# Kernel optimization log

Measured on AMD Instinct MI355X. Metric: run time of the kernel, lower is better.

Reference implementation:

```python
import jax, jax.numpy as jnp
import numpy as np

H = 90            # hidden_size (hard-coded in module)
NODE_F = 16       # conv1 in_channels = dim(x) + dim(pos)
EDGE_F = 8
N_GRAPHS = 512


def _init_linear(key, fan_in, fan_out):
    kw, kb = jax.random.split(key)
    bound = 1.0 / np.sqrt(fan_in)
    w = jax.random.uniform(kw, (fan_in, fan_out), minval=-bound, maxval=bound, dtype=jnp.float32)
    b = jax.random.uniform(kb, (fan_out,), minval=-bound, maxval=bound, dtype=jnp.float32)
    return w, b


def setup_inputs() -> dict:
    key = jax.random.key(0)
    ks = jax.random.split(key, 16)
    N, E = 16000, 64000
    x = jax.random.normal(ks[0], (N, 13), dtype=jnp.float32)
    pos = jax.random.normal(ks[1], (N, 3), dtype=jnp.float32)
    edge_attr = jax.random.normal(ks[2], (E, EDGE_F), dtype=jnp.float32)
    edge_index = jax.random.randint(ks[3], (2, E), 0, N, dtype=jnp.int32)
    batch = jnp.sort(jax.random.randint(ks[4], (N,), 0, N_GRAPHS, dtype=jnp.int32))

    # conv1: edge MLP edge_f -> H -> NODE_F*H ; root [NODE_F,H]; bias [H]
    c1_w1, c1_b1 = _init_linear(ks[5], EDGE_F, H)
    c1_w2, c1_b2 = _init_linear(ks[6], H, NODE_F * H)
    c1_root = jax.random.normal(ks[7], (NODE_F, H), dtype=jnp.float32) / np.sqrt(NODE_F)
    c1_bias = jnp.zeros((H,), dtype=jnp.float32)
    # conv2: H -> H
    c2_w1, c2_b1 = _init_linear(ks[8], EDGE_F, H)
    c2_w2, c2_b2 = _init_linear(ks[9], H, H * H)
    c2_root = jax.random.normal(ks[10], (H, H), dtype=jnp.float32) / np.sqrt(H)
    c2_bias = jnp.zeros((H,), dtype=jnp.float32)
    # conv3: H -> H//2
    c3_w1, c3_b1 = _init_linear(ks[11], EDGE_F, H)
    c3_w2, c3_b2 = _init_linear(ks[12], H, H * (H // 2))
    c3_root = jax.random.normal(ks[13], (H, H // 2), dtype=jnp.float32) / np.sqrt(H)
    c3_bias = jnp.zeros((H // 2,), dtype=jnp.float32)

    fc1_w, fc1_b = _init_linear(ks[14], H // 2, H)
    out_w, out_b = _init_linear(ks[15], H, 1)

    return dict(x=x, pos=pos, edge_attr=edge_attr, edge_index=edge_index, batch=batch,
                c1_w1=c1_w1, c1_b1=c1_b1, c1_w2=c1_w2, c1_b2=c1_b2, c1_root=c1_root, c1_bias=c1_bias,
                c2_w1=c2_w1, c2_b1=c2_b1, c2_w2=c2_w2, c2_b2=c2_b2, c2_root=c2_root, c2_bias=c2_bias,
                c3_w1=c3_w1, c3_b1=c3_b1, c3_w2=c3_w2, c3_b2=c3_b2, c3_root=c3_root, c3_bias=c3_bias,
                fc1_w=fc1_w, fc1_b=fc1_b, out_w=out_w, out_b=out_b)


def _nnconv(x, src, dst, edge_attr, w1, b1, w2, b2, root, bias, in_c, out_c):
    # edge MLP -> per-edge weight matrix theta[e] in R^{in_c x out_c}
    h = jax.nn.relu(edge_attr @ w1 + b1)                  # [E, H]
    theta = (h @ w2 + b2).reshape(-1, in_c, out_c)        # [E, in_c, out_c]
    msg = jnp.einsum('ei,eio->eo', x[src], theta)         # gather + per-edge matvec
    agg = jax.ops.segment_sum(msg, dst, num_segments=x.shape[0])  # scatter-add
    return agg + x @ root + bias


def reference(x, pos, edge_attr, edge_index, batch,
              c1_w1, c1_b1, c1_w2, c1_b2, c1_root, c1_bias,
              c2_w1, c2_b1, c2_w2, c2_b2, c2_root, c2_bias,
              c3_w1, c3_b1, c3_w2, c3_b2, c3_root, c3_bias,
              fc1_w, fc1_b, out_w, out_b):
    src, dst = edge_index[0], edge_index[1]
    h = jnp.concatenate([x, pos], axis=1)                 # [N, NODE_F]
    h = jax.nn.relu(_nnconv(h, src, dst, edge_attr, c1_w1, c1_b1, c1_w2, c1_b2, c1_root, c1_bias, NODE_F, H))
    h = jax.nn.relu(_nnconv(h, src, dst, edge_attr, c2_w1, c2_b1, c2_w2, c2_b2, c2_root, c2_bias, H, H))
    h = jax.nn.relu(_nnconv(h, src, dst, edge_attr, c3_w1, c3_b1, c3_w2, c3_b2, c3_root, c3_bias, H, H // 2))
    g = jax.ops.segment_sum(h, batch, num_segments=N_GRAPHS)  # global_add_pool
    g = jax.nn.relu(g @ fc1_w + fc1_b)
    return g @ out_w + out_b                               # [N_GRAPHS, 1]
```

## Files before the change

kernel.cpp:

```cpp
#include <hip/hip_runtime.h>

#define NN 16000
#define NE 64000
#define HD 90
#define NG 512

typedef float f32x4 __attribute__((ext_vector_type(4)));
typedef float f32x16 __attribute__((ext_vector_type(16)));
typedef short s16x8 __attribute__((ext_vector_type(8)));

__device__ __forceinline__ unsigned short rhu1(float f) {
  return (unsigned short)((__builtin_bit_cast(unsigned int, f) + 0x8000u) >> 16);
}
__device__ __forceinline__ unsigned int rhu_pack(float lo, float hi) {
  unsigned int ul = __builtin_bit_cast(unsigned int, lo) + 0x8000u;
  unsigned int uh = __builtin_bit_cast(unsigned int, hi) + 0x8000u;
  return __builtin_amdgcn_perm(uh, ul, 0x07060302u);
}
__device__ __forceinline__ float bfhi(unsigned int u) {
  return __builtin_bit_cast(float, u & 0xFFFF0000u);
}
__device__ __forceinline__ float bflo(unsigned int u) {
  return __builtin_bit_cast(float, u << 16);
}

__global__ void concat_kernel(const float* __restrict__ x, const float* __restrict__ pos,
                              float* __restrict__ h0) {
  int idx = blockIdx.x * 256 + threadIdx.x;
  if (idx >= NN * 16) return;
  int n = idx >> 4, c = idx & 15;
  h0[idx] = (c < 13) ? x[n * 13 + c] : pos[n * 3 + (c - 13)];
}

__global__ void edge_mlp_bf(const float* __restrict__ ea, const float* __restrict__ w1,
                            const float* __restrict__ b1, unsigned short* __restrict__ he) {
  int idx = blockIdx.x * 256 + threadIdx.x;
  if (idx >= NE * 96) return;
  int e = idx / 96, k = idx - e * 96;
  unsigned short v;
  if (k < 90) {
    const float* a = ea + e * 8;
    float acc = b1[k];
#pragma unroll
    for (int j = 0; j < 8; j++) acc = fmaf(a[j], w1[j * HD + k], acc);
    v = rhu1(fmaxf(acc, 0.f));
  } else {
    v = (k == 90) ? (unsigned short)0x3F80 : (unsigned short)0;
  }
  he[idx] = v;
}

template <int OC, int NOT>
__global__ void wprep_frag32(const float* __restrict__ w2, const float* __restrict__ b2,
                             unsigned short* __restrict__ wout, int inc_oc) {
  const int i = blockIdx.x;
  unsigned int* wo = (unsigned int*)(wout + (size_t)i * NOT * 6 * 512);
  for (int u = threadIdx.x; u < NOT * 6 * 256; u += 256) {
    int f = u >> 8, r = u & 255;
    int ot = f / 6;
    int c = f - 6 * ot;
    int lane = r >> 2, uu = r & 3;
    int o = ot * 32 + (lane & 31);
    int hk = c * 16 + ((lane >> 5) << 3) + 2 * uu;
    float v0 = 0.f, v1 = 0.f;
    if (o < OC) {
      if (hk < 90) v0 = w2[hk * inc_oc + i * OC + o];
      else if (hk == 90) v0 = b2[i * OC + o];
      int hk1 = hk + 1;
      if (hk1 < 90) v1 = w2[hk1 * inc_oc + i * OC + o];
      else if (hk1 == 90) v1 = b2[i * OC + o];
    }
    wo[u] = rhu_pack(v0, v1);
  }
}

#define LOADB(II, B)                                                           \
  do {                                                                         \
    const unsigned short* wg_ = wl + ((size_t)((II) * NOT + wn) * 6 + kh3) * 512; \
    B[0] = *(const s16x8*)(wg_);                                               \
    B[1] = *(const s16x8*)(wg_ + 512);                                         \
    B[2] = *(const s16x8*)(wg_ + 1024);                                        \
  } while (0)

#define BODY(II, B)                                                            \
  do {                                                                         \
    _Pragma("unroll")                                                          \
    for (int mt = 0; mt < 2; mt++) {                                           \
      const int zbase = (II) * 64 + mt * 32 + h * 16;                          \
      const uint4 za = *(const uint4*)&zb[zbase];                              \
      const uint4 zc = *(const uint4*)&zb[zbase + 8];                          \
      f32x16 t = __builtin_amdgcn_mfma_f32_32x32x16_bf16(af[mt][0], B[0], (f32x16)0.f, 0, 0, 0); \
      t = __builtin_amdgcn_mfma_f32_32x32x16_bf16(af[mt][1], B[1], t, 0, 0, 0);\
      t = __builtin_amdgcn_mfma_f32_32x32x16_bf16(af[mt][2], B[2], t, 0, 0, 0);\
      f32x16 zv;                                                               \
      zv[0] = bflo(za.x);  zv[1] = bfhi(za.x);  zv[2] = bflo(za.y);  zv[3] = bfhi(za.y); \
      zv[4] = bflo(za.z);  zv[5] = bfhi(za.z);  zv[6] = bflo(za.w);  zv[7] = bfhi(za.w); \
      zv[8] = bflo(zc.x);  zv[9] = bfhi(zc.x);  zv[10] = bflo(zc.y); zv[11] = bfhi(zc.y); \
      zv[12] = bflo(zc.z); zv[13] = bfhi(zc.z); zv[14] = bflo(zc.w); zv[15] = bfhi(zc.w); \
      acc[mt] += zv * t;                                                       \
    }                                                                          \
  } while (0)

template <int ILIM, int OC, int NOT, int BLK>
__global__ __launch_bounds__(BLK, 3)
void msg_mfma(const unsigned short* __restrict__ he,
              const float* __restrict__ nin,
              const int* __restrict__ src, const int* __restrict__ dst,
              const unsigned short* __restrict__ wp,
              float* __restrict__ agg) {
  __shared__ unsigned short zb[ILIM * 64];
  __shared__ float mrg[NOT * 64 * 32];
  __shared__ int dst_s[64];
  const int tid = threadIdx.x;
  const int e0 = blockIdx.x * 64;
  const int wid = tid >> 6, l = tid & 63, ln32 = l & 31, h = l >> 5;
  const int kh = wid & 1, wn = wid >> 1;
  const int kh3 = kh * 3;

  if (tid < 64) dst_s[tid] = dst[e0 + tid];

  {
    const int e = tid & 63, jj = tid >> 6;
    const int pe = ((e >> 5) << 5) + (((e >> 2) & 1) << 4) + (((e >> 3) & 3) << 2) + (e & 3);
    const float* zr = nin + (size_t)src[e0 + e] * ILIM;
    for (int p = jj; p < ILIM / 2; p += NOT * 2) {
      const float2 v = *(const float2*)(zr + 2 * p);
      zb[(2 * p) * 64 + pe] = rhu1(v.x);
      zb[(2 * p + 1) * 64 + pe] = rhu1(v.y);
    }
  }

  s16x8 af[2][3];
#pragma unroll
  for (int mt = 0; mt < 2; mt++) {
    const unsigned short* hr = he + (size_t)(e0 + mt * 32 + ln32) * 96 + kh * 48 + h * 8;
#pragma unroll
    for (int c = 0; c < 3; c++) af[mt][c] = *(const s16x8*)(hr + c * 16);
  }

  const unsigned short* wl = wp + l * 8;
  s16x8 b0[3], b1[3];
  LOADB(0, b0);

  __syncthreads();

  f32x16 acc[2];
  acc[0] = (f32x16)0.f;
  acc[1] = (f32x16)0.f;

#pragma clang loop unroll(disable)
  for (int i = 0; i < ILIM; i += 2) {
    if (i + 1 < ILIM) LOADB(i + 1, b1);
    BODY(i, b0);
    if (i + 1 < ILIM) {
      if (i + 2 < ILIM) LOADB(i + 2, b0);
      BODY(i + 1, b1);
    }
  }

  if (kh) {
    float* mr = &mrg[wn * 2048];
#pragma unroll
    for (int mt = 0; mt < 2; mt++)
#pragma unroll
      for (int r = 0; r < 16; r++) {
        int row = (r & 3) + 8 * (r >> 2) + 4 * h;
        mr[(mt * 32 + row) * 32 + ln32] = acc[mt][r];
      }
  }
  __syncthreads();
  if (!kh) {
    const int o = wn * 32 + ln32;
    if (o < OC) {
      const float* mr = &mrg[wn * 2048];
#pragma unroll
      for (int mt = 0; mt < 2; mt++)
#pragma unroll
        for (int r = 0; r < 16; r++) {
          int row = (r & 3) + 8 * (r >> 2) + 4 * h;
          int el = mt * 32 + row;
          atomicAdd(agg + (size_t)dst_s[el] * OC + o, acc[mt][r] + mr[el * 32 + ln32]);
        }
    }
  }
}

template <int IN_C, int OC>
__global__ void node_kernel(const float* __restrict__ agg, const float* __restrict__ nin,
                            const float* __restrict__ root, const float* __restrict__ bias,
                            float* __restrict__ out) {
  int idx = blockIdx.x * 256 + threadIdx.x;
  if (idx >= NN * OC) return;
  int n = idx / OC, o = idx - n * OC;
  float acc = agg[idx] + bias[o];
  const float* inp = nin + (size_t)n * IN_C;
#pragma unroll 6
  for (int i = 0; i < IN_C; i++) acc = fmaf(inp[i], root[i * OC + o], acc);
  out[idx] = fmaxf(acc, 0.f);
}

__global__ void pool_mlp_kernel(const float* __restrict__ h3, const int* __restrict__ batch,
                                const float* __restrict__ fc1_w, const float* __restrict__ fc1_b,
                                const float* __restrict__ out_w, const float* __restrict__ out_b,
                                float* __restrict__ out) {
  const int b = blockIdx.x;
  const int tid = threadIdx.x;
  __shared__ float g[45];
  __shared__ float go[90];
  __shared__ int rng[2];
  if (tid < 2) {
    int target = b + tid;
    int lo = 0, hi = NN;
    while (lo < hi) { int mid = (lo + hi) >> 1; if (batch[mid] < target) lo = mid + 1; else hi = mid; }
    rng[tid] = lo;
  }
  __syncthreads();
  const int s = rng[0], e = rng[1];
  if (tid < 45) {
    float acc = 0.f;
    for (int n = s; n < e; n++) acc += h3[n * 45 + tid];
    g[tid] = acc;
  }
  __syncthreads();
  if (tid < 90) {
    float acc = fc1_b[tid];
#pragma unroll 5
    for (int i = 0; i < 45; i++) acc = fmaf(g[i], fc1_w[i * 90 + tid], acc);
    go[tid] = fmaxf(acc, 0.f) * out_w[tid];
  }
  __syncthreads();
  if (tid == 0) {
    float acc = out_b[0];
    for (int i = 0; i < 90; i++) acc += go[i];
    out[b] = acc;
  }
}

extern "C" void kernel_launch(void* const* d_in, const int* in_sizes, int n_in,
                              void* d_out, int out_size, void* d_ws, size_t ws_size,
                              hipStream_t stream) {
  const float* x       = (const float*)d_in[0];
  const float* pos     = (const float*)d_in[1];
  const float* ea      = (const float*)d_in[2];
  const int*   eidx    = (const int*)d_in[3];
  const int*   batch   = (const int*)d_in[4];
  const float* c1_w1   = (const float*)d_in[5];
  const float* c1_b1   = (const float*)d_in[6];
  const float* c1_w2   = (const float*)d_in[7];
  const float* c1_b2   = (const float*)d_in[8];
  const float* c1_root = (const float*)d_in[9];
  const float* c1_bias = (const float*)d_in[10];
  const float* c2_w1   = (const float*)d_in[11];
  const float* c2_b1   = (const float*)d_in[12];
  const float* c2_w2   = (const float*)d_in[13];
  const float* c2_b2   = (const float*)d_in[14];
  const float* c2_root = (const float*)d_in[15];
  const float* c2_bias = (const float*)d_in[16];
  const float* c3_w1   = (const float*)d_in[17];
  const float* c3_b1   = (const float*)d_in[18];
  const float* c3_w2   = (const float*)d_in[19];
  const float* c3_b2   = (const float*)d_in[20];
  const float* c3_root = (const float*)d_in[21];
  const float* c3_bias = (const float*)d_in[22];
  const float* fc1_w   = (const float*)d_in[23];
  const float* fc1_b   = (const float*)d_in[24];
  const float* out_w   = (const float*)d_in[25];
  const float* out_b   = (const float*)d_in[26];
  const int* src = eidx;
  const int* dst = eidx + NE;

  float* ws  = (float*)d_ws;
  float* h0  = ws;
  float* h1  = h0 + NN * 16;
  float* h2  = h1 + NN * 90;
  float* h3  = h2 + NN * 90;
  float* agg = h3 + NN * 45;
  unsigned short* he_bf = (unsigned short*)(agg + NN * 90);
  unsigned short* wp1 = he_bf + (size_t)NE * 96;
  unsigned short* wp2 = wp1 + (size_t)16 * 3 * 6 * 512;
  unsigned short* wp3 = wp2 + (size_t)90 * 3 * 6 * 512;

  concat_kernel<<<(NN * 16) / 256, 256, 0, stream>>>(x, pos, h0);

  wprep_frag32<90, 3><<<16, 256, 0, stream>>>(c1_w2, c1_b2, wp1, 16 * 90);
  wprep_frag32<90, 3><<<90, 256, 0, stream>>>(c2_w2, c2_b2, wp2, 90 * 90);
  wprep_frag32<45, 2><<<90, 256, 0, stream>>>(c3_w2, c3_b2, wp3, 90 * 45);

  hipMemsetAsync(agg, 0, (size_t)NN * 90 * sizeof(float), stream);
  edge_mlp_bf<<<(NE * 96) / 256, 256, 0, stream>>>(ea, c1_w1, c1_b1, he_bf);
  msg_mfma<16, 90, 3, 384><<<NE / 64, 384, 0, stream>>>(he_bf, h0, src, dst, wp1, agg);
  node_kernel<16, 90><<<(NN * 90) / 256, 256, 0, stream>>>(agg, h0, c1_root, c1_bias, h1);

  hipMemsetAsync(agg, 0, (size_t)NN * 90 * sizeof(float), stream);
  edge_mlp_bf<<<(NE * 96) / 256, 256, 0, stream>>>(ea, c2_w1, c2_b1, he_bf);
  msg_mfma<90, 90, 3, 384><<<NE / 64, 384, 0, stream>>>(he_bf, h1, src, dst, wp2, agg);
  node_kernel<90, 90><<<(NN * 90) / 256, 256, 0, stream>>>(agg, h1, c2_root, c2_bias, h2);

  hipMemsetAsync(agg, 0, (size_t)NN * 45 * sizeof(float), stream);
  edge_mlp_bf<<<(NE * 96) / 256, 256, 0, stream>>>(ea, c3_w1, c3_b1, he_bf);
  msg_mfma<90, 45, 2, 256><<<NE / 64, 256, 0, stream>>>(he_bf, h2, src, dst, wp3, agg);
  node_kernel<90, 45><<<(NN * 45 + 255) / 256, 256, 0, stream>>>(agg, h2, c3_root, c3_bias, h3);

  pool_mlp_kernel<<<NG, 128, 0, stream>>>(h3, batch, fc1_w, fc1_b, out_w, out_b, (float*)d_out);
}
```

Before: 601.3 us.

## Alias z-buffer and merge scratch in LDS and triple-buffer B loads

The per-edge z staging buffer and the split-K merge buffer now share one LDS allocation, and the merge is done one M-tile at a time with extra barriers, which shrinks shared memory per block. The B-fragment prefetch goes from two to three register buffers so loads run further ahead of the MFMA chain. The goal is higher occupancy and better latency hiding of weight loads. The cost is more registers, which could spill under the launch bound of 3, plus extra synchronisation in the epilogue.

```diff
diff --git a/kernel.cpp b/kernel.cpp
--- a/kernel.cpp
+++ b/kernel.cpp
@@ -108,9 +108,12 @@
               const int* __restrict__ src, const int* __restrict__ dst,
               const unsigned short* __restrict__ wp,
               float* __restrict__ agg) {
-  __shared__ unsigned short zb[ILIM * 64];
-  __shared__ float mrg[NOT * 64 * 32];
+  constexpr int ZBYTES = ILIM * 64 * 2;
+  constexpr int MBYTES = NOT * 32 * 32 * 4;
+  constexpr int SBYTES = (ZBYTES > MBYTES ? ZBYTES : MBYTES);
+  __shared__ char smem[SBYTES];
   __shared__ int dst_s[64];
+  unsigned short* zb = (unsigned short*)smem;
   const int tid = threadIdx.x;
   const int e0 = blockIdx.x * 64;
   const int wid = tid >> 6, l = tid & 63, ln32 = l & 31, h = l >> 5;
@@ -139,8 +142,9 @@
   }
 
   const unsigned short* wl = wp + l * 8;
-  s16x8 b0[3], b1[3];
+  s16x8 b0[3], b1[3], b2[3];
   LOADB(0, b0);
+  if (ILIM > 1) LOADB(1, b1);
 
   __syncthreads();
 
@@ -149,39 +153,43 @@
   acc[1] = (f32x16)0.f;
 
 #pragma clang loop unroll(disable)
-  for (int i = 0; i < ILIM; i += 2) {
-    if (i + 1 < ILIM) LOADB(i + 1, b1);
+  for (int i = 0; i < ILIM; i += 3) {
+    if (i + 2 < ILIM) LOADB(i + 2, b2);
     BODY(i, b0);
     if (i + 1 < ILIM) {
-      if (i + 2 < ILIM) LOADB(i + 2, b0);
+      if (i + 3 < ILIM) LOADB(i + 3, b0);
       BODY(i + 1, b1);
-    }
-  }
-
-  if (kh) {
-    float* mr = &mrg[wn * 2048];
-#pragma unroll
-    for (int mt = 0; mt < 2; mt++)
+      if (i + 2 < ILIM) {
+        if (i + 4 < ILIM) LOADB(i + 4, b1);
+        BODY(i + 2, b2);
+      }
+    }
+  }
+
+  __syncthreads();
+  float* mrg = (float*)smem;
+#pragma unroll
+  for (int mt = 0; mt < 2; mt++) {
+    if (kh) {
 #pragma unroll
       for (int r = 0; r < 16; r++) {
         int row = (r & 3) + 8 * (r >> 2) + 4 * h;
-        mr[(mt * 32 + row) * 32 + ln32] = acc[mt][r];
+        mrg[(wn * 32 + row) * 32 + ln32] = acc[mt][r];
       }
-  }
-  __syncthreads();
-  if (!kh) {
-    const int o = wn * 32 + ln32;
-    if (o < OC) {
-      const float* mr = &mrg[wn * 2048];
-#pragma unroll
-      for (int mt = 0; mt < 2; mt++)
+    }
+    __syncthreads();
+    if (!kh) {
+      const int o = wn * 32 + ln32;
+      if (o < OC) {
 #pragma unroll
         for (int r = 0; r < 16; r++) {
           int row = (r & 3) + 8 * (r >> 2) + 4 * h;
-          int el = mt * 32 + row;
-          atomicAdd(agg + (size_t)dst_s[el] * OC + o, acc[mt][r] + mr[el * 32 + ln32]);
+          atomicAdd(agg + (size_t)dst_s[mt * 32 + row] * OC + o,
+                    acc[mt][r] + mrg[(wn * 32 + row) * 32 + ln32]);
         }
-    }
+      }
+    }
+    __syncthreads();
   }
 }
 
```

New measurement: 1.150 ms. 91.3% more time.
